# Kernel optimization log

Measured on AMD Instinct MI355X. Metric: run time of the kernel, lower is better.

## Reference

```python
import jax, jax.numpy as jnp
import numpy as np

N = 50000   # num_entities
E = 600000  # num_edges
D = 128     # dim
R = 200     # num_relations
T = 1000    # num_timestamps
L = 2       # num_layers


def setup_inputs() -> dict:
    key = jax.random.key(0)
    ks = jax.random.split(key, 16)
    edge_index = jax.random.randint(ks[0], (2, E), 0, N)
    edge_type = jax.random.randint(ks[1], (E,), 0, R)
    edge_time = jax.random.randint(ks[2], (E,), 0, T)
    edge_weight = jax.random.uniform(ks[3], (E,), dtype=jnp.float32)
    perm = jax.random.permutation(ks[4], N)
    entity_emb = jax.random.normal(ks[5], (N, D), dtype=jnp.float32)
    rel_emb = jax.random.normal(ks[6], (R, D), dtype=jnp.float32)
    time_emb = jax.random.normal(ks[7], (T, D), dtype=jnp.float32)
    s = 1.0 / np.sqrt(D)
    in_proj_w = jax.random.uniform(ks[8], (L, D, 2 * D), minval=-s, maxval=s)
    in_proj_b = jax.random.uniform(ks[9], (L, 2 * D), minval=-s, maxval=s)
    out_proj_w = jax.random.uniform(ks[10], (L, D, D), minval=-s, maxval=s)
    out_proj_b = jax.random.uniform(ks[11], (L, D), minval=-s, maxval=s)
    A = jax.random.normal(ks[12], (L, D)) * 0.1
    B = jax.random.normal(ks[13], (L, D)) * 0.1
    ln_g = jnp.ones((L, D), dtype=jnp.float32)
    ln_b = jnp.zeros((L, D), dtype=jnp.float32)
    return dict(edge_index=edge_index, edge_type=edge_type, edge_time=edge_time,
                edge_weight=edge_weight, perm=perm, entity_emb=entity_emb,
                rel_emb=rel_emb, time_emb=time_emb, in_proj_w=in_proj_w,
                in_proj_b=in_proj_b, out_proj_w=out_proj_w, out_proj_b=out_proj_b,
                A=A, B=B, ln_g=ln_g, ln_b=ln_b)


def _mamba_layer(x, Wi, bi, Wo, bo, A, B, g_ln, b_ln):
    # x: [N, D]
    zg = x @ Wi + bi                      # [N, 2D]
    z, g = jnp.split(zg, 2, axis=-1)
    g = jax.nn.sigmoid(g)

    def step(prev, zg_i):
        z_i, g_i = zg_i
        curr = g_i * (A * prev) + B * z_i
        return curr, curr

    _, h = jax.lax.scan(step, jnp.zeros((D,), x.dtype), (z, g))  # [N, D]
    y = x + h @ Wo + bo
    mu = jnp.mean(y, axis=-1, keepdims=True)
    var = jnp.mean((y - mu) ** 2, axis=-1, keepdims=True)
    return (y - mu) / jnp.sqrt(var + 1e-5) * g_ln + b_ln


def reference(edge_index, edge_type, edge_time, edge_weight, perm, entity_emb,
              rel_emb, time_emb, in_proj_w, in_proj_b, out_proj_w, out_proj_b,
              A, B, ln_g, ln_b):
    src, dst = edge_index[0], edge_index[1]
    msgs = entity_emb[src] + rel_emb[edge_type] + time_emb[edge_time]  # [E, D]
    sums = jax.ops.segment_sum(msgs * edge_weight[:, None], dst, num_segments=N)
    cnt = jax.ops.segment_sum(edge_weight, dst, num_segments=N)
    x = sums / jnp.maximum(cnt, 1.0)[:, None]          # scatter_mean
    x = x / jnp.maximum(jnp.linalg.norm(x, axis=1, keepdims=True), 1e-12)
    x = x[perm]
    for l in range(L):
        x = _mamba_layer(x, in_proj_w[l], in_proj_b[l], out_proj_w[l],
                         out_proj_b[l], A[l], B[l], ln_g[l], ln_b[l])
    return x
```

## Files before the change

### kernel.cpp

```cpp
#include <hip/hip_runtime.h>
#include <hip/hip_bf16.h>

typedef unsigned short ushort_t;
typedef unsigned int   uint_t;
typedef __attribute__((ext_vector_type(8))) short bf8;
typedef __attribute__((ext_vector_type(4))) float f32x4;

constexpr int N = 50000;
constexpr int E = 600000;
constexpr int D = 128;
constexpr int L = 2;
constexpr int NB = (N + 255) / 256;

constexpr int RB   = 80;
constexpr int RBLK = N / RB;
constexpr int LOOK = 16;
constexpr int HSTR = 136;

__device__ __forceinline__ float us2f(ushort_t u) {
    union { uint_t i; float f; } c; c.i = (uint_t)u << 16; return c.f;
}
__device__ __forceinline__ float u2f(uint_t u) {
    union { uint_t i; float f; } c; c.i = u; return c.f;
}
__device__ __forceinline__ ushort_t f2us(float f) {
    __hip_bfloat16 b = __float2bfloat16(f);
    return *(ushort_t*)&b;
}

__global__ __launch_bounds__(256) void k_alloc(
    const int* __restrict__ hist, int* __restrict__ gcnt,
    int* __restrict__ cursor, int* __restrict__ rowst)
{
    int i = blockIdx.x * 256 + threadIdx.x;
    int v = (i < N) ? hist[i] : 0;
    int lane = threadIdx.x & 63;
    int s = v;
    #pragma unroll
    for (int m = 1; m < 64; m <<= 1) {
        int t = __shfl_up(s, m, 64);
        if (lane >= m) s += t;
    }
    int base = 0;
    if (lane == 63) base = atomicAdd(gcnt, s);
    base = __shfl(base, 63, 64);
    int b = base + s - v;
    if (i < N) {
        cursor[i] = b;
        rowst[i]  = b;
    }
}

__global__ __launch_bounds__(256) void k_scatter(
    const int* __restrict__ eidx, const int* __restrict__ etype,
    const int* __restrict__ etime, const float* __restrict__ ew,
    int* __restrict__ cursor, int2* __restrict__ esort)
{
    int e = blockIdx.x * 256 + threadIdx.x;
    if (e >= E) return;
    int dst = eidx[E + e];
    int slot = atomicAdd(&cursor[dst], 1);
    int2 p;
    p.x = (eidx[e] & 0xffff) | (etype[e] << 16);
    p.y = (etime[e] & 0xffff) | ((int)f2us(ew[e]) << 16);
    esort[slot] = p;
}

constexpr size_t CAST_TBL = 3276800;
constexpr size_t CAST_W   = CAST_TBL + (size_t)L * 256 * 128
                                     + (size_t)L * 128 * 128;
constexpr size_t CAST_H   = CAST_W + E;
constexpr size_t CAST_TOT = CAST_H + N;

__global__ __launch_bounds__(256) void k_cast(
    const float* __restrict__ ent, const float* __restrict__ rel,
    const float* __restrict__ tim, const float* __restrict__ Wi,
    const float* __restrict__ Wo, const int* __restrict__ dstp,
    const int* __restrict__ perm,
    ushort_t* __restrict__ entb, ushort_t* __restrict__ relb,
    ushort_t* __restrict__ timb, ushort_t* __restrict__ WiT,
    ushort_t* __restrict__ WoT, int* __restrict__ hist,
    int* __restrict__ invp)
{
    size_t t = (size_t)blockIdx.x * 256 + threadIdx.x;
    if (t < CAST_TBL) {
        const float2* s; uint_t* d; size_t off;
        if (t < 3200000)      { s = (const float2*)ent; d = (uint_t*)entb; off = t; }
        else if (t < 3212800) { s = (const float2*)rel; d = (uint_t*)relb; off = t - 3200000; }
        else                  { s = (const float2*)tim; d = (uint_t*)timb; off = t - 3212800; }
        float2 v = s[off];
        d[off] = (uint_t)f2us(v.x) | ((uint_t)f2us(v.y) << 16);
    } else if (t < CAST_W) {
        size_t u = t - CAST_TBL;
        if (u < (size_t)L * 256 * 128) {
            int l = u / (256 * 128), r = u % (256 * 128);
            int n = r / 128, k = r % 128;
            WiT[u] = f2us(Wi[(size_t)l * 128 * 256 + k * 256 + n]);
        } else {
            size_t v = u - (size_t)L * 256 * 128;
            int l = v / (128 * 128), r = v % (128 * 128);
            int n = r / 128, k = r % 128;
            WoT[v] = f2us(Wo[(size_t)l * 128 * 128 + k * 128 + n]);
        }
    } else if (t < CAST_H) {
        int e = (int)(t - CAST_W);
        atomicAdd(&hist[dstp[e]], 1);
    } else if (t < CAST_TOT) {
        int i = (int)(t - CAST_H);
        invp[perm[i]] = i;
    }
}

__global__ __launch_bounds__(256) void k_agg(
    const int2* __restrict__ esort, const int* __restrict__ rowst,
    const int* __restrict__ hist, const int* __restrict__ invp,
    const ushort_t* __restrict__ entb, const ushort_t* __restrict__ relb,
    const ushort_t* __restrict__ timb, ushort_t* __restrict__ xbf)
{
    int wv = threadIdx.x >> 6, lane = threadIdx.x & 63;
    int d = blockIdx.x * 4 + wv;
    if (d >= N) return;
    int beg = __builtin_amdgcn_readfirstlane(rowst[d]);
    int n   = __builtin_amdgcn_readfirstlane(hist[d]);

    const uint_t* entu = (const uint_t*)entb;
    const uint_t* relu = (const uint_t*)relb;
    const uint_t* timu = (const uint_t*)timb;

    float s0[4] = {0.f, 0.f, 0.f, 0.f};
    float s1[4] = {0.f, 0.f, 0.f, 0.f};
    float wacc = 0.f;

    for (int c0 = 0; c0 < n; c0 += 64) {
        int mm = n - c0; if (mm > 64) mm = 64;
        int2 rec = esort[beg + c0 + lane];
        uint_t recx = (uint_t)rec.x, recy = (uint_t)rec.y;
        wacc += (lane < mm) ? u2f(recy & 0xffff0000u) : 0.f;

        int j = 0;
        for (; j + 3 < mm; j += 4) {
            #pragma unroll
            for (int u = 0; u < 4; u++) {
                uint_t rx = (uint_t)__builtin_amdgcn_readlane((int)recx, j + u);
                uint_t ry = (uint_t)__builtin_amdgcn_readlane((int)recy, j + u);
                const uint_t* pe = entu + ((size_t)(rx & 0xffffu) << 6);
                const uint_t* pr = relu + ((size_t)(rx >> 16) << 6);
                const uint_t* pt = timu + ((size_t)(ry & 0xffffu) << 6);
                float w = u2f(ry & 0xffff0000u);
                uint_t va = pe[lane];
                uint_t vb = pr[lane];
                uint_t vc = pt[lane];
                float lo = (u2f(va << 16) + u2f(vb << 16)) + u2f(vc << 16);
                float hi = (u2f(va & 0xffff0000u) + u2f(vb & 0xffff0000u))
                         + u2f(vc & 0xffff0000u);
                s0[u] = fmaf(lo, w, s0[u]);
                s1[u] = fmaf(hi, w, s1[u]);
            }
        }
        for (; j < mm; j++) {
            uint_t rx = (uint_t)__builtin_amdgcn_readlane((int)recx, j);
            uint_t ry = (uint_t)__builtin_amdgcn_readlane((int)recy, j);
            const uint_t* pe = entu + ((size_t)(rx & 0xffffu) << 6);
            const uint_t* pr = relu + ((size_t)(rx >> 16) << 6);
            const uint_t* pt = timu + ((size_t)(ry & 0xffffu) << 6);
            float w = u2f(ry & 0xffff0000u);
            uint_t va = pe[lane];
            uint_t vb = pr[lane];
            uint_t vc = pt[lane];
            float lo = (u2f(va << 16) + u2f(vb << 16)) + u2f(vc << 16);
            float hi = (u2f(va & 0xffff0000u) + u2f(vb & 0xffff0000u))
                     + u2f(vc & 0xffff0000u);
            s0[0] = fmaf(lo, w, s0[0]);
            s1[0] = fmaf(hi, w, s1[0]);
        }
    }
    float a0 = (s0[0] + s0[1]) + (s0[2] + s0[3]);
    float a1 = (s1[0] + s1[1]) + (s1[2] + s1[3]);

    float wsum = wacc;
    #pragma unroll
    for (int m = 32; m >= 1; m >>= 1) wsum += __shfl_xor(wsum, m, 64);

    float inv = 1.0f / fmaxf(wsum, 1.0f);
    a0 *= inv; a1 *= inv;

    float ss = a0 * a0 + a1 * a1;
    #pragma unroll
    for (int m = 32; m >= 1; m >>= 1) ss += __shfl_xor(ss, m, 64);
    float sc = 1.0f / fmaxf(sqrtf(ss), 1e-12f);

    int orow = invp[d];
    uint_t out = (uint_t)f2us(a0 * sc) | ((uint_t)f2us(a1 * sc) << 16);
    *(uint_t*)(xbf + (size_t)orow * D + 2 * lane) = out;
}

__global__ __launch_bounds__(256, 4) void k_zg(
    const ushort_t* __restrict__ xin, const ushort_t* __restrict__ WiT,
    const float* __restrict__ bi, const float* __restrict__ Aw,
    const float* __restrict__ Bw, uint_t* __restrict__ coeff)
{
    int tid = threadIdx.x;
    int w = tid >> 6, lane = tid & 63;
    int quad = lane >> 4, m = lane & 15;
    int r0 = blockIdx.x * RB;

    int cz0 = w * 32 + m;
    int cz1 = cz0 + 16;

    float Ad0 = Aw[cz0], Bd0 = Bw[cz0];
    float Ad1 = Aw[cz1], Bd1 = Bw[cz1];
    float bz0 = bi[cz0], bz1 = bi[cz1];
    float bg0 = bi[cz0 + 128], bg1 = bi[cz1 + 128];

    const f32x4 zero4 = {0.f, 0.f, 0.f, 0.f};

    bf8 Bz0[4], Bz1[4], Bg0[4], Bg1[4];
    #pragma unroll
    for (int kb = 0; kb < 4; kb++) {
        int ko = kb * 32 + quad * 8;
        Bz0[kb] = *(const bf8*)(WiT + (size_t)cz0 * 128 + ko);
        Bz1[kb] = *(const bf8*)(WiT + (size_t)cz1 * 128 + ko);
        Bg0[kb] = *(const bf8*)(WiT + (size_t)(cz0 + 128) * 128 + ko);
        Bg1[kb] = *(const bf8*)(WiT + (size_t)(cz1 + 128) * 128 + ko);
    }

    #pragma unroll
    for (int rt = 0; rt < RB / 16; rt++) {
        bf8 a[4];
        #pragma unroll
        for (int kb = 0; kb < 4; kb++)
            a[kb] = *(const bf8*)(xin + (size_t)(r0 + rt * 16 + m) * 128
                                       + kb * 32 + quad * 8);
        f32x4 az0 = zero4, az1 = zero4, ag0 = zero4, ag1 = zero4;
        #pragma unroll
        for (int kb = 0; kb < 4; kb++) {
            az0 = __builtin_amdgcn_mfma_f32_16x16x32_bf16(a[kb], Bz0[kb], az0, 0, 0, 0);
            az1 = __builtin_amdgcn_mfma_f32_16x16x32_bf16(a[kb], Bz1[kb], az1, 0, 0, 0);
            ag0 = __builtin_amdgcn_mfma_f32_16x16x32_bf16(a[kb], Bg0[kb], ag0, 0, 0, 0);
            ag1 = __builtin_amdgcn_mfma_f32_16x16x32_bf16(a[kb], Bg1[kb], ag1, 0, 0, 0);
        }
        #pragma unroll
        for (int reg = 0; reg < 4; reg++) {
            int row = r0 + rt * 16 + quad * 4 + reg;
            float z0 = az0[reg] + bz0, z1 = az1[reg] + bz1;
            float g0 = 1.f / (1.f + __expf(-(ag0[reg] + bg0)));
            float g1 = 1.f / (1.f + __expf(-(ag1[reg] + bg1)));
            uint_t p0 = (uint_t)f2us(g0 * Ad0) | ((uint_t)f2us(Bd0 * z0) << 16);
            uint_t p1 = (uint_t)f2us(g1 * Ad1) | ((uint_t)f2us(Bd1 * z1) << 16);
            coeff[(size_t)row * 128 + cz0] = p0;
            coeff[(size_t)row * 128 + cz1] = p1;
        }
    }
}

template <bool FINAL>
__global__ __launch_bounds__(256, 4) void k_scanout(
    const uint_t* __restrict__ coeff, const ushort_t* __restrict__ xin,
    const ushort_t* __restrict__ WoT, const float* __restrict__ bo,
    const float* __restrict__ lg, const float* __restrict__ lb,
    ushort_t* __restrict__ xoutb, float* __restrict__ outf)
{
    __shared__ ushort_t hs[RB * HSTR];
    __shared__ float redS[16 * 4], redQ[16 * 4], muA[16], rsA[16];

    int tid = threadIdx.x;
    int w = tid >> 6, lane = tid & 63;
    int quad = lane >> 4, m = lane & 15;
    int r0 = blockIdx.x * RB;

    int c0 = w * 32 + m, c1 = c0 + 16;

    bf8 b0[4], b1[4];
    #pragma unroll
    for (int kb = 0; kb < 4; kb++) {
        int ko = kb * 32 + quad * 8;
        b0[kb] = *(const bf8*)(WoT + (size_t)c0 * 128 + ko);
        b1[kb] = *(const bf8*)(WoT + (size_t)c1 * 128 + ko);
    }
    float bias0 = bo[c0], bias1 = bo[c1];
    float gl0 = lg[c0], gl1 = lg[c1], bl0 = lb[c0], bl1 = lb[c1];

    if (tid < 128) {
        float h = 0.f;
        #pragma unroll
        for (int i = 0; i < LOOK; i++) {
            int row = r0 - LOOK + i;
            int rc = row < 0 ? 0 : row;
            uint_t c = coeff[(size_t)rc * 128 + tid];
            float ca = us2f((ushort_t)(c & 0xffff));
            float cb = us2f((ushort_t)(c >> 16));
            h = (row >= 0) ? fmaf(ca, h, cb) : 0.f;
        }
        #pragma unroll 8
        for (int i = 0; i < RB; i++) {
            uint_t c = coeff[(size_t)(r0 + i) * 128 + tid];
            float ca = us2f((ushort_t)(c & 0xffff));
            float cb = us2f((ushort_t)(c >> 16));
            h = fmaf(ca, h, cb);
            hs[i * HSTR + tid] = f2us(h);
        }
    }
    __syncthreads();

    for (int rt = 0; rt < RB / 16; rt++) {
        bf8 a[4];
        #pragma unroll
        for (int kb = 0; kb < 4; kb++)
            a[kb] = *(const bf8*)(hs + (rt * 16 + m) * HSTR + kb * 32 + quad * 8);
        f32x4 acc0 = {0.f, 0.f, 0.f, 0.f}, acc1 = acc0;
        #pragma unroll
        for (int kb = 0; kb < 4; kb++) {
            acc0 = __builtin_amdgcn_mfma_f32_16x16x32_bf16(a[kb], b0[kb], acc0, 0, 0, 0);
            acc1 = __builtin_amdgcn_mfma_f32_16x16x32_bf16(a[kb], b1[kb], acc1, 0, 0, 0);
        }
        float y0[4], y1[4];
        #pragma unroll
        for (int reg = 0; reg < 4; reg++) {
            int gr = r0 + rt * 16 + quad * 4 + reg;
            y0[reg] = acc0[reg] + bias0 + us2f(xin[(size_t)gr * 128 + c0]);
            y1[reg] = acc1[reg] + bias1 + us2f(xin[(size_t)gr * 128 + c1]);
        }
        #pragma unroll
        for (int reg = 0; reg < 4; reg++) {
            float v0 = y0[reg], v1 = y1[reg];
            float s = v0 + v1, q = v0 * v0 + v1 * v1;
            #pragma unroll
            for (int mk = 1; mk <= 8; mk <<= 1) {
                s += __shfl_xor(s, mk, 64);
                q += __shfl_xor(q, mk, 64);
            }
            if (m == 0) {
                int row = quad * 4 + reg;
                redS[row * 4 + w] = s;
                redQ[row * 4 + w] = q;
            }
        }
        __syncthreads();
        if (tid < 16) {
            float s = redS[tid * 4] + redS[tid * 4 + 1] + redS[tid * 4 + 2] + redS[tid * 4 + 3];
            float q = redQ[tid * 4] + redQ[tid * 4 + 1] + redQ[tid * 4 + 2] + redQ[tid * 4 + 3];
            float mu = s * (1.f / 128.f);
            float var = q * (1.f / 128.f) - mu * mu;
            muA[tid] = mu;
            rsA[tid] = rsqrtf(var + 1e-5f);
        }
        __syncthreads();
        #pragma unroll
        for (int reg = 0; reg < 4; reg++) {
            int rr = quad * 4 + reg;
            int gr = r0 + rt * 16 + rr;
            float mu = muA[rr], rs = rsA[rr];
            float v0 = (y0[reg] - mu) * rs * gl0 + bl0;
            float v1 = (y1[reg] - mu) * rs * gl1 + bl1;
            if (FINAL) {
                outf[(size_t)gr * 128 + c0] = v0;
                outf[(size_t)gr * 128 + c1] = v1;
            } else {
                xoutb[(size_t)gr * 128 + c0] = f2us(v0);
                xoutb[(size_t)gr * 128 + c1] = f2us(v1);
            }
        }
    }
}

extern "C" void kernel_launch(void* const* d_in, const int* in_sizes, int n_in,
                              void* d_out, int out_size, void* d_ws, size_t ws_size,
                              hipStream_t stream)
{
    const int*   eidx  = (const int*)d_in[0];
    const int*   etype = (const int*)d_in[1];
    const int*   etime = (const int*)d_in[2];
    const float* ew    = (const float*)d_in[3];
    const int*   perm  = (const int*)d_in[4];
    const float* ent   = (const float*)d_in[5];
    const float* rel   = (const float*)d_in[6];
    const float* tim   = (const float*)d_in[7];
    const float* Wi    = (const float*)d_in[8];
    const float* bi    = (const float*)d_in[9];
    const float* Wo    = (const float*)d_in[10];
    const float* bo    = (const float*)d_in[11];
    const float* Aw    = (const float*)d_in[12];
    const float* Bw    = (const float*)d_in[13];
    const float* lg    = (const float*)d_in[14];
    const float* lbp   = (const float*)d_in[15];

    char* base = (char*)d_ws;
    size_t o = 0;
    ushort_t* xbf  = (ushort_t*)(base + o); o += (size_t)N * D * 2;
    ushort_t* xb2  = (ushort_t*)(base + o); o += (size_t)N * D * 2;
    ushort_t* entb = (ushort_t*)(base + o); o += (size_t)N * D * 2;
    ushort_t* relb = (ushort_t*)(base + o); o += (size_t)200 * D * 2;
    ushort_t* timb = (ushort_t*)(base + o); o += (size_t)1000 * D * 2;
    ushort_t* WiT  = (ushort_t*)(base + o); o += (size_t)L * 256 * 128 * 2;
    ushort_t* WoT  = (ushort_t*)(base + o); o += (size_t)L * 128 * 128 * 2;
    int2*     esort  = (int2*)(base + o);   o += (size_t)E * 8;
    int*      hist   = (int*)(base + o);    o += (size_t)N * 4;
    int*      gcnt   = (int*)(base + o);    o += 4;
    int*      cursor = (int*)(base + o);    o += (size_t)N * 4;
    int*      rowst  = (int*)(base + o);    o += (size_t)N * 4;
    int*      invp   = (int*)(base + o);    o += (size_t)N * 4;
    uint_t*   coeff  = (uint_t*)(base + o); o += (size_t)N * D * 4;

    hipMemsetAsync(hist, 0, (N + 1) * sizeof(int), stream);

    k_cast    <<<(int)((CAST_TOT + 255) / 256), 256, 0, stream>>>(
                  ent, rel, tim, Wi, Wo, eidx + E, perm,
                  entb, relb, timb, WiT, WoT, hist, invp);
    k_alloc   <<<NB, 256, 0, stream>>>(hist, gcnt, cursor, rowst);
    k_scatter <<<(E + 255) / 256, 256, 0, stream>>>(eidx, etype, etime, ew,
                                                    cursor, esort);
    k_agg     <<<(N + 3) / 4, 256, 0, stream>>>(esort, rowst, hist, invp,
                                                entb, relb, timb, xbf);

    k_zg<<<RBLK, 256, 0, stream>>>(xbf, WiT, bi, Aw, Bw, coeff);
    k_scanout<false><<<RBLK, 256, 0, stream>>>(coeff, xbf, WoT, bo, lg, lbp,
                                               xb2, nullptr);
    k_zg<<<RBLK, 256, 0, stream>>>(xb2, WiT + (size_t)256 * 128, bi + 256,
                                   Aw + 128, Bw + 128, coeff);
    k_scanout<true><<<RBLK, 256, 0, stream>>>(coeff, xb2,
                                              WoT + (size_t)128 * 128, bo + 128,
                                              lg + 128, lbp + 128,
                                              nullptr, (float*)d_out);
}
```

Before: 294.5 us.

## Fuse in-projection, scan and out-projection into one per-layer kernel via LDS

Merges the zg and scan/out kernels into a single per-layer kernel that writes gate/input coefficients to shared memory instead of a global coeff buffer. Each block recomputes the 16-row lookahead halo of the in-projection GEMM so the chunked scan can run locally. This removes a global write and read of an N×128×4-byte buffer per layer plus one launch per layer. The cost is extra MFMA work on the halo rows, more shared memory per block, and a lower occupancy bound (2 blocks).

```diff
diff --git a/kernel.cpp b/kernel.cpp
--- a/kernel.cpp
+++ b/kernel.cpp
@@ -15,7 +15,8 @@
 constexpr int RB   = 80;
 constexpr int RBLK = N / RB;
 constexpr int LOOK = 16;
-constexpr int HSTR = 136;
+constexpr int CSTR = 136;
+constexpr int CROWS = RB + LOOK;
 
 __device__ __forceinline__ float us2f(ushort_t u) {
     union { uint_t i; float f; } c; c.i = (uint_t)u << 16; return c.f;
@@ -194,18 +195,25 @@
     *(uint_t*)(xbf + (size_t)orow * D + 2 * lane) = out;
 }
 
-__global__ __launch_bounds__(256, 4) void k_zg(
+template <bool FINAL>
+__global__ __launch_bounds__(256, 2) void k_layer(
     const ushort_t* __restrict__ xin, const ushort_t* __restrict__ WiT,
-    const float* __restrict__ bi, const float* __restrict__ Aw,
-    const float* __restrict__ Bw, uint_t* __restrict__ coeff)
-{
+    const float* __restrict__ bi, const ushort_t* __restrict__ WoT,
+    const float* __restrict__ bo, const float* __restrict__ Aw,
+    const float* __restrict__ Bw, const float* __restrict__ lg,
+    const float* __restrict__ lb, ushort_t* __restrict__ xoutb,
+    float* __restrict__ outf)
+{
+    __shared__ ushort_t SCA[CROWS * CSTR];
+    __shared__ ushort_t SCB[CROWS * CSTR];
+    __shared__ float redS[16 * 4], redQ[16 * 4], muA[16], rsA[16];
+
     int tid = threadIdx.x;
     int w = tid >> 6, lane = tid & 63;
     int quad = lane >> 4, m = lane & 15;
     int r0 = blockIdx.x * RB;
 
-    int cz0 = w * 32 + m;
-    int cz1 = cz0 + 16;
+    int cz0 = w * 32 + m, cz1 = cz0 + 16;
 
     float Ad0 = Aw[cz0], Bd0 = Bw[cz0];
     float Ad1 = Aw[cz1], Bd1 = Bw[cz1];
@@ -225,12 +233,13 @@
     }
 
     #pragma unroll
-    for (int rt = 0; rt < RB / 16; rt++) {
+    for (int rt = 0; rt < CROWS / 16; rt++) {
+        int gr = r0 - LOOK + rt * 16 + m;
+        int grc = gr < 0 ? 0 : gr;
         bf8 a[4];
         #pragma unroll
         for (int kb = 0; kb < 4; kb++)
-            a[kb] = *(const bf8*)(xin + (size_t)(r0 + rt * 16 + m) * 128
-                                       + kb * 32 + quad * 8);
+            a[kb] = *(const bf8*)(xin + (size_t)grc * 128 + kb * 32 + quad * 8);
         f32x4 az0 = zero4, az1 = zero4, ag0 = zero4, ag1 = zero4;
         #pragma unroll
         for (int kb = 0; kb < 4; kb++) {
@@ -241,72 +250,53 @@
         }
         #pragma unroll
         for (int reg = 0; reg < 4; reg++) {
-            int row = r0 + rt * 16 + quad * 4 + reg;
+            int lr = rt * 16 + quad * 4 + reg;
             float z0 = az0[reg] + bz0, z1 = az1[reg] + bz1;
             float g0 = 1.f / (1.f + __expf(-(ag0[reg] + bg0)));
             float g1 = 1.f / (1.f + __expf(-(ag1[reg] + bg1)));
-            uint_t p0 = (uint_t)f2us(g0 * Ad0) | ((uint_t)f2us(Bd0 * z0) << 16);
-            uint_t p1 = (uint_t)f2us(g1 * Ad1) | ((uint_t)f2us(Bd1 * z1) << 16);
-            coeff[(size_t)row * 128 + cz0] = p0;
-            coeff[(size_t)row * 128 + cz1] = p1;
-        }
-    }
-}
-
-template <bool FINAL>
-__global__ __launch_bounds__(256, 4) void k_scanout(
-    const uint_t* __restrict__ coeff, const ushort_t* __restrict__ xin,
-    const ushort_t* __restrict__ WoT, const float* __restrict__ bo,
-    const float* __restrict__ lg, const float* __restrict__ lb,
-    ushort_t* __restrict__ xoutb, float* __restrict__ outf)
-{
-    __shared__ ushort_t hs[RB * HSTR];
-    __shared__ float redS[16 * 4], redQ[16 * 4], muA[16], rsA[16];
-
-    int tid = threadIdx.x;
-    int w = tid >> 6, lane = tid & 63;
-    int quad = lane >> 4, m = lane & 15;
-    int r0 = blockIdx.x * RB;
-
-    int c0 = w * 32 + m, c1 = c0 + 16;
+            SCA[lr * CSTR + cz0] = f2us(g0 * Ad0);
+            SCB[lr * CSTR + cz0] = f2us(Bd0 * z0);
+            SCA[lr * CSTR + cz1] = f2us(g1 * Ad1);
+            SCB[lr * CSTR + cz1] = f2us(Bd1 * z1);
+        }
+    }
+    __syncthreads();
+
+    if (tid < 128) {
+        float h = 0.f;
+        #pragma unroll
+        for (int i = 0; i < LOOK; i++) {
+            int row = r0 - LOOK + i;
+            float ca = us2f(SCA[i * CSTR + tid]);
+            float cb = us2f(SCB[i * CSTR + tid]);
+            h = (row >= 0) ? fmaf(ca, h, cb) : 0.f;
+        }
+        #pragma unroll 8
+        for (int i = LOOK; i < CROWS; i++) {
+            float ca = us2f(SCA[i * CSTR + tid]);
+            float cb = us2f(SCB[i * CSTR + tid]);
+            h = fmaf(ca, h, cb);
+            SCA[i * CSTR + tid] = f2us(h);
+        }
+    }
+    __syncthreads();
 
     bf8 b0[4], b1[4];
     #pragma unroll
     for (int kb = 0; kb < 4; kb++) {
         int ko = kb * 32 + quad * 8;
-        b0[kb] = *(const bf8*)(WoT + (size_t)c0 * 128 + ko);
-        b1[kb] = *(const bf8*)(WoT + (size_t)c1 * 128 + ko);
-    }
-    float bias0 = bo[c0], bias1 = bo[c1];
-    float gl0 = lg[c0], gl1 = lg[c1], bl0 = lb[c0], bl1 = lb[c1];
-
-    if (tid < 128) {
-        float h = 0.f;
-        #pragma unroll
-        for (int i = 0; i < LOOK; i++) {
-            int row = r0 - LOOK + i;
-            int rc = row < 0 ? 0 : row;
-            uint_t c = coeff[(size_t)rc * 128 + tid];
-            float ca = us2f((ushort_t)(c & 0xffff));
-            float cb = us2f((ushort_t)(c >> 16));
-            h = (row >= 0) ? fmaf(ca, h, cb) : 0.f;
-        }
-        #pragma unroll 8
-        for (int i = 0; i < RB; i++) {
-            uint_t c = coeff[(size_t)(r0 + i) * 128 + tid];
-            float ca = us2f((ushort_t)(c & 0xffff));
-            float cb = us2f((ushort_t)(c >> 16));
-            h = fmaf(ca, h, cb);
-            hs[i * HSTR + tid] = f2us(h);
-        }
-    }
-    __syncthreads();
+        b0[kb] = *(const bf8*)(WoT + (size_t)cz0 * 128 + ko);
+        b1[kb] = *(const bf8*)(WoT + (size_t)cz1 * 128 + ko);
+    }
+    float bias0 = bo[cz0], bias1 = bo[cz1];
+    float gl0 = lg[cz0], gl1 = lg[cz1], bl0 = lb[cz0], bl1 = lb[cz1];
 
     for (int rt = 0; rt < RB / 16; rt++) {
         bf8 a[4];
         #pragma unroll
         for (int kb = 0; kb < 4; kb++)
-            a[kb] = *(const bf8*)(hs + (rt * 16 + m) * HSTR + kb * 32 + quad * 8);
+            a[kb] = *(const bf8*)(SCA + (LOOK + rt * 16 + m) * CSTR
+                                      + kb * 32 + quad * 8);
         f32x4 acc0 = {0.f, 0.f, 0.f, 0.f}, acc1 = acc0;
         #pragma unroll
         for (int kb = 0; kb < 4; kb++) {
@@ -317,8 +307,8 @@
         #pragma unroll
         for (int reg = 0; reg < 4; reg++) {
             int gr = r0 + rt * 16 + quad * 4 + reg;
-            y0[reg] = acc0[reg] + bias0 + us2f(xin[(size_t)gr * 128 + c0]);
-            y1[reg] = acc1[reg] + bias1 + us2f(xin[(size_t)gr * 128 + c1]);
+            y0[reg] = acc0[reg] + bias0 + us2f(xin[(size_t)gr * 128 + cz0]);
+            y1[reg] = acc1[reg] + bias1 + us2f(xin[(size_t)gr * 128 + cz1]);
         }
         #pragma unroll
         for (int reg = 0; reg < 4; reg++) {
@@ -353,11 +343,11 @@
             float v0 = (y0[reg] - mu) * rs * gl0 + bl0;
             float v1 = (y1[reg] - mu) * rs * gl1 + bl1;
             if (FINAL) {
-                outf[(size_t)gr * 128 + c0] = v0;
-                outf[(size_t)gr * 128 + c1] = v1;
+                outf[(size_t)gr * 128 + cz0] = v0;
+                outf[(size_t)gr * 128 + cz1] = v1;
             } else {
-                xoutb[(size_t)gr * 128 + c0] = f2us(v0);
-                xoutb[(size_t)gr * 128 + c1] = f2us(v1);
+                xoutb[(size_t)gr * 128 + cz0] = f2us(v0);
+                xoutb[(size_t)gr * 128 + cz1] = f2us(v1);
             }
         }
     }
@@ -399,7 +389,6 @@
     int*      cursor = (int*)(base + o);    o += (size_t)N * 4;
     int*      rowst  = (int*)(base + o);    o += (size_t)N * 4;
     int*      invp   = (int*)(base + o);    o += (size_t)N * 4;
-    uint_t*   coeff  = (uint_t*)(base + o); o += (size_t)N * D * 4;
 
     hipMemsetAsync(hist, 0, (N + 1) * sizeof(int), stream);
 
@@ -412,13 +401,10 @@
     k_agg     <<<(N + 3) / 4, 256, 0, stream>>>(esort, rowst, hist, invp,
                                                 entb, relb, timb, xbf);
 
-    k_zg<<<RBLK, 256, 0, stream>>>(xbf, WiT, bi, Aw, Bw, coeff);
-    k_scanout<false><<<RBLK, 256, 0, stream>>>(coeff, xbf, WoT, bo, lg, lbp,
-                                               xb2, nullptr);
-    k_zg<<<RBLK, 256, 0, stream>>>(xb2, WiT + (size_t)256 * 128, bi + 256,
-                                   Aw + 128, Bw + 128, coeff);
-    k_scanout<true><<<RBLK, 256, 0, stream>>>(coeff, xb2,
-                                              WoT + (size_t)128 * 128, bo + 128,
-                                              lg + 128, lbp + 128,
-                                              nullptr, (float*)d_out);
-}
+    k_layer<false><<<RBLK, 256, 0, stream>>>(
+        xbf, WiT, bi, WoT, bo, Aw, Bw, lg, lbp, xb2, nullptr);
+    k_layer<true><<<RBLK, 256, 0, stream>>>(
+        xb2, WiT + (size_t)256 * 128, bi + 256, WoT + (size_t)128 * 128,
+        bo + 128, Aw + 128, Bw + 128, lg + 128, lbp + 128,
+        nullptr, (float*)d_out);
+}
```

Result: faster. 283.9 us (-3.6%).
